# Optimization experiments

Measured on AMD Instinct MI355X. Metric: run time of the kernel, lower is better.

## Reference

```python
import jax, jax.numpy as jnp
import numpy as np

B, F, V, E = 16384, 39, 100000, 16
D0, D1, D2 = 32, 32, 32

def setup_inputs() -> dict:
    key = jax.random.key(0)
    ks = jax.random.split(key, 12)
    return {
        "Xi": jax.random.randint(ks[0], (B, F, 1), 0, V),
        "Xv": jax.random.uniform(ks[1], (B, F), dtype=jnp.float32),
        "emb_tables": jax.random.normal(ks[2], (F, V, E), dtype=jnp.float32),
        "w_first": jax.random.normal(ks[3], (D0, F, E), dtype=jnp.float32),
        "w_inner": jax.random.normal(ks[4], (D0, F, E), dtype=jnp.float32),
        "lin1_W": jax.random.normal(ks[5], (D1, D0), dtype=jnp.float32) * 0.1,
        "lin1_b": jax.random.normal(ks[6], (D1,), dtype=jnp.float32) * 0.1,
        "lin2_W": jax.random.normal(ks[7], (D2, D1), dtype=jnp.float32) * 0.1,
        "lin2_b": jax.random.normal(ks[8], (D2,), dtype=jnp.float32) * 0.1,
        "last_W": jax.random.normal(ks[9], (1, D2), dtype=jnp.float32) * 0.1,
        "last_b": jax.random.normal(ks[10], (1,), dtype=jnp.float32) * 0.1,
    }

def reference(Xi, Xv, emb_tables, w_first, w_inner, lin1_W, lin1_b, lin2_W, lin2_b, last_W, last_b):
    idx = Xi[:, :, 0]                                  # [B,F]
    # per-field embedding gather, scaled by feature value
    emb = emb_tables[jnp.arange(F)[None, :], idx]      # [B,F,E]
    emb = emb * Xv[:, :, None]                         # [B,F,E]
    # first-order: nested loops over (D0, F) collapse to one einsum
    first = jnp.einsum('bfe,dfe->bd', emb, w_first)    # [B,D0]
    # inner-product second-order: (sum over fields of <emb_f, w_df>)^2
    s = jnp.einsum('bfe,dfe->bd', emb, w_inner)        # [B,D0]
    x = first + s * s
    # deep MLP (relu, no dropout/batchnorm in inference)
    x = jax.nn.relu(x @ lin1_W.T + lin1_b)
    x = jax.nn.relu(x @ lin2_W.T + lin2_b)
    x = x @ last_W.T + last_b                          # [B,1]
    return jnp.sum(x, axis=1)                          # [B]
```

## Files before the change

### kernel.cpp

```cpp
#include <hip/hip_runtime.h>


namespace {

typedef _Float16 half8 __attribute__((ext_vector_type(8)));
typedef float floatx4 __attribute__((ext_vector_type(4)));

constexpr int Bn = 16384;
constexpr int Fn = 39;
constexpr int Vn = 100000;
constexpr int En = 16;
constexpr int M = 32;
constexpr int KST = 20;
constexpr int NRT = Bn / 16;
constexpr int WBLOCKS = 20;
constexpr int AWS_OFF_H = 65536;

__device__ __forceinline__ half8 cvt8s(float4 a, float4 b, float s) {
    half8 h;
    h[0] = (_Float16)(a.x * s); h[1] = (_Float16)(a.y * s);
    h[2] = (_Float16)(a.z * s); h[3] = (_Float16)(a.w * s);
    h[4] = (_Float16)(b.x * s); h[5] = (_Float16)(b.y * s);
    h[6] = (_Float16)(b.z * s); h[7] = (_Float16)(b.w * s);
    return h;
}

__device__ __forceinline__ half8 cvt8(float4 a, float4 b) {
    half8 h;
    h[0] = (_Float16)a.x; h[1] = (_Float16)a.y;
    h[2] = (_Float16)a.z; h[3] = (_Float16)a.w;
    h[4] = (_Float16)b.x; h[5] = (_Float16)b.y;
    h[6] = (_Float16)b.z; h[7] = (_Float16)b.w;
    return h;
}

__global__ __launch_bounds__(256) void pnn_stage(
    const int* __restrict__ Xi,
    const float* __restrict__ Xv,
    const float* __restrict__ T,
    const float* __restrict__ w_first,
    const float* __restrict__ w_inner,
    _Float16* __restrict__ ws)
{
    _Float16* __restrict__ Wws = ws;
    _Float16* __restrict__ Aws = ws + AWS_OFF_H;

    const int tid = threadIdx.x;

    if (blockIdx.x >= NRT) {
        const int slot = (blockIdx.x - NRT) * 256 + tid;
        const int t16 = slot / (KST * 64);
        const int rem = slot % (KST * 64);
        const int t = rem >> 6;
        const int lane = rem & 63;
        const int n = t16 * 16 + (lane & 15);
        const int kb = t * 32 + (lane >> 4) * 8;
        half8 h = {0, 0, 0, 0, 0, 0, 0, 0};
        if (!(t == KST - 1 && (lane >> 4) >= 2)) {
            const float* src = ((n < 32) ? (w_first + (size_t)n * 624)
                                         : (w_inner + (size_t)(n - 32) * 624)) + kb;
            const float4 a = *reinterpret_cast<const float4*>(src);
            const float4 b = *reinterpret_cast<const float4*>(src + 4);
            h = cvt8(a, b);
        }
        *reinterpret_cast<half8*>(Wws + (size_t)slot * 8) = h;
        return;
    }

    __shared__ _Float16 At[KST * 512];
    __shared__ int   xi[624];
    __shared__ float xv[624];

    const int rt = blockIdx.x;
    const int r0 = rt * 16;

    if (tid < 156) {
        reinterpret_cast<int4*>(xi)[tid] =
            reinterpret_cast<const int4*>(Xi + (size_t)r0 * Fn)[tid];
        reinterpret_cast<float4*>(xv)[tid] =
            reinterpret_cast<const float4*>(Xv + (size_t)r0 * Fn)[tid];
    }
    if (tid < 32) {
        half8 z = {0, 0, 0, 0, 0, 0, 0, 0};
        *reinterpret_cast<half8*>(At + ((KST - 1) * 64 + 32 + tid) * 8) = z;
    }
    __syncthreads();

    for (int i = tid; i < 624; i += 256) {
        const int r = i & 15, f = i >> 4;
        const int idx = xi[r * Fn + f];
        const float s = xv[r * Fn + f];
        const float4* src = reinterpret_cast<const float4*>(
            T + ((size_t)f * Vn + (size_t)idx) * En);
        const float4 q0 = src[0], q1 = src[1], q2 = src[2], q3 = src[3];
        const int base = (((f >> 1) * 64) + (f & 1) * 32 + r) * 8;
        *reinterpret_cast<half8*>(At + base)       = cvt8s(q0, q1, s);
        *reinterpret_cast<half8*>(At + base + 128) = cvt8s(q2, q3, s);
    }
    __syncthreads();

    const int4* s4 = reinterpret_cast<const int4*>(At);
    int4* d4 = reinterpret_cast<int4*>(Aws + (size_t)rt * KST * 512);
#pragma unroll
    for (int j = 0; j < 5; ++j) d4[tid + j * 256] = s4[tid + j * 256];
}

struct SMemE {
    float x[M * 69];
    float wsh[2176];
    float r1[1024];
    float r2[1024];
};

__global__ __launch_bounds__(512) void pnn_gemm(
    const _Float16* __restrict__ ws,
    const float* __restrict__ lin1_W,
    const float* __restrict__ lin1_b,
    const float* __restrict__ lin2_W,
    const float* __restrict__ lin2_b,
    const float* __restrict__ last_W,
    const float* __restrict__ last_b,
    float* __restrict__ out)
{
    __shared__ SMemE sm;

    const _Float16* __restrict__ Wws = ws;
    const _Float16* __restrict__ Aws = ws + AWS_OFF_H;

    const int tid = threadIdx.x;
    const int lane = tid & 63;
    const int wv = tid >> 6;
    const int q = wv & 1;
    const int t16 = wv >> 1;
    const int row0 = blockIdx.x * M;

    const _Float16* aptr = Aws + ((size_t)(blockIdx.x * 2 + q) * KST) * 512 + lane * 8;
    const _Float16* bptr = Wws + ((size_t)t16 * KST) * 512 + lane * 8;

    floatx4 acc = {0.0f, 0.0f, 0.0f, 0.0f};
#pragma unroll
    for (int t = 0; t < KST; ++t) {
        const half8 af = *reinterpret_cast<const half8*>(aptr + t * 512);
        const half8 bf = *reinterpret_cast<const half8*>(bptr + t * 512);
        acc = __builtin_amdgcn_mfma_f32_16x16x32_f16(af, bf, acc, 0, 0, 0);
    }

    {
        const int col = t16 * 16 + (lane & 15);
        const int rbase = q * 16 + (lane >> 4) * 4;
#pragma unroll
        for (int r = 0; r < 4; ++r)
            sm.x[(rbase + r) * 69 + col] = acc[r];
    }

    for (int i = tid; i < 2145; i += 512) {
        float v;
        if (i < 1024)      v = lin1_W[i];
        else if (i < 2048) v = lin2_W[i - 1024];
        else if (i < 2080) v = lin1_b[i - 2048];
        else if (i < 2112) v = lin2_b[i - 2080];
        else if (i < 2144) v = last_W[i - 2112];
        else               v = last_b[0];
        sm.wsh[i] = v;
    }
    __syncthreads();

    for (int p = tid; p < 1024; p += 512) {
        const int j = p >> 5, r = p & 31;
        const float fi = sm.x[r * 69 + j];
        const float s  = sm.x[r * 69 + 32 + j];
        sm.r1[j * 32 + r] = fi + s * s;
    }
    __syncthreads();

    {
        const int r = tid & 31, n0 = (tid >> 5) * 2;
        float a0 = sm.wsh[2048 + n0];
        float a1 = sm.wsh[2048 + n0 + 1];
#pragma unroll
        for (int j = 0; j < 32; ++j) {
            const float xj = sm.r1[j * 32 + r];
            a0 = fmaf(sm.wsh[n0 * 32 + j],       xj, a0);
            a1 = fmaf(sm.wsh[(n0 + 1) * 32 + j], xj, a1);
        }
        sm.r2[n0 * 32 + r]       = fmaxf(a0, 0.0f);
        sm.r2[(n0 + 1) * 32 + r] = fmaxf(a1, 0.0f);
    }
    __syncthreads();

    {
        const int r = tid & 31, n0 = (tid >> 5) * 2;
        float a0 = sm.wsh[2080 + n0];
        float a1 = sm.wsh[2080 + n0 + 1];
#pragma unroll
        for (int j = 0; j < 32; ++j) {
            const float xj = sm.r2[j * 32 + r];
            a0 = fmaf(sm.wsh[1024 + n0 * 32 + j],       xj, a0);
            a1 = fmaf(sm.wsh[1024 + (n0 + 1) * 32 + j], xj, a1);
        }
        sm.r1[n0 * 32 + r]       = fmaxf(a0, 0.0f);
        sm.r1[(n0 + 1) * 32 + r] = fmaxf(a1, 0.0f);
    }
    __syncthreads();

    if (tid < M) {
        float res = sm.wsh[2144];
#pragma unroll
        for (int j = 0; j < 32; ++j)
            res = fmaf(sm.wsh[2112 + j], sm.r1[j * 32 + tid], res);
        out[row0 + tid] = res;
    }
}

}

extern "C" void kernel_launch(void* const* d_in, const int* in_sizes, int n_in,
                              void* d_out, int out_size, void* d_ws, size_t ws_size,
                              hipStream_t stream) {
    (void)in_sizes; (void)n_in; (void)out_size; (void)ws_size;
    const int*   Xi      = (const int*)d_in[0];
    const float* Xv      = (const float*)d_in[1];
    const float* T       = (const float*)d_in[2];
    const float* w_first = (const float*)d_in[3];
    const float* w_inner = (const float*)d_in[4];
    const float* lin1_W  = (const float*)d_in[5];
    const float* lin1_b  = (const float*)d_in[6];
    const float* lin2_W  = (const float*)d_in[7];
    const float* lin2_b  = (const float*)d_in[8];
    const float* last_W  = (const float*)d_in[9];
    const float* last_b  = (const float*)d_in[10];
    float* out = (float*)d_out;
    _Float16* ws = (_Float16*)d_ws;

    hipLaunchKernelGGL(pnn_stage, dim3(NRT + WBLOCKS), dim3(256), 0, stream,
                       Xi, Xv, T, w_first, w_inner, ws);
    hipLaunchKernelGGL(pnn_gemm, dim3(Bn / M), dim3(512), 0, stream,
                       ws, lin1_W, lin1_b, lin2_W, lin2_b, last_W, last_b, out);
}
```

Before: 330.4 us.

## Gather embeddings one thread per (row, field) writing directly to workspace

Replaces the per-16-row block that staged the embedding gather through shared memory with a flat grid where each thread handles one (batch row, field) pair and writes its scaled fp16 fragments straight into the MFMA-ready workspace layout. Table reads use nontemporal loads, and the zero padding of the last K step moves into separate zero-fill blocks. This removes the shared-memory staging, the barriers and the limited per-block parallelism. In exchange the Xi/Xv reads are strided across threads and the global stores are scattered 16-byte writes.

```diff
diff --git a/kernel.cpp b/kernel.cpp
--- a/kernel.cpp
+++ b/kernel.cpp
@@ -5,6 +5,7 @@
 
 typedef _Float16 half8 __attribute__((ext_vector_type(8)));
 typedef float floatx4 __attribute__((ext_vector_type(4)));
+typedef float f32x4 __attribute__((ext_vector_type(4)));
 
 constexpr int Bn = 16384;
 constexpr int Fn = 39;
@@ -12,18 +13,11 @@
 constexpr int En = 16;
 constexpr int M = 32;
 constexpr int KST = 20;
-constexpr int NRT = Bn / 16;
+constexpr int AWS_OFF_H = 65536;
+
+constexpr int GB = (Bn * Fn) / 256;
 constexpr int WBLOCKS = 20;
-constexpr int AWS_OFF_H = 65536;
-
-__device__ __forceinline__ half8 cvt8s(float4 a, float4 b, float s) {
-    half8 h;
-    h[0] = (_Float16)(a.x * s); h[1] = (_Float16)(a.y * s);
-    h[2] = (_Float16)(a.z * s); h[3] = (_Float16)(a.w * s);
-    h[4] = (_Float16)(b.x * s); h[5] = (_Float16)(b.y * s);
-    h[6] = (_Float16)(b.z * s); h[7] = (_Float16)(b.w * s);
-    return h;
-}
+constexpr int ZBLOCKS = 128;
 
 __device__ __forceinline__ half8 cvt8(float4 a, float4 b) {
     half8 h;
@@ -31,6 +25,15 @@
     h[2] = (_Float16)a.z; h[3] = (_Float16)a.w;
     h[4] = (_Float16)b.x; h[5] = (_Float16)b.y;
     h[6] = (_Float16)b.z; h[7] = (_Float16)b.w;
+    return h;
+}
+
+__device__ __forceinline__ half8 cvt8s(f32x4 a, f32x4 b, float s) {
+    half8 h;
+    h[0] = (_Float16)(a[0] * s); h[1] = (_Float16)(a[1] * s);
+    h[2] = (_Float16)(a[2] * s); h[3] = (_Float16)(a[3] * s);
+    h[4] = (_Float16)(b[0] * s); h[5] = (_Float16)(b[1] * s);
+    h[6] = (_Float16)(b[2] * s); h[7] = (_Float16)(b[3] * s);
     return h;
 }
 
@@ -46,63 +49,55 @@
     _Float16* __restrict__ Aws = ws + AWS_OFF_H;
 
     const int tid = threadIdx.x;
-
-    if (blockIdx.x >= NRT) {
-        const int slot = (blockIdx.x - NRT) * 256 + tid;
-        const int t16 = slot / (KST * 64);
-        const int rem = slot % (KST * 64);
-        const int t = rem >> 6;
-        const int lane = rem & 63;
-        const int n = t16 * 16 + (lane & 15);
-        const int kb = t * 32 + (lane >> 4) * 8;
-        half8 h = {0, 0, 0, 0, 0, 0, 0, 0};
-        if (!(t == KST - 1 && (lane >> 4) >= 2)) {
-            const float* src = ((n < 32) ? (w_first + (size_t)n * 624)
-                                         : (w_inner + (size_t)(n - 32) * 624)) + kb;
-            const float4 a = *reinterpret_cast<const float4*>(src);
-            const float4 b = *reinterpret_cast<const float4*>(src + 4);
-            h = cvt8(a, b);
+    const int blk = blockIdx.x;
+
+    if (blk >= GB) {
+        if (blk < GB + WBLOCKS) {
+            const int slot = (blk - GB) * 256 + tid;
+            const int t16 = slot / (KST * 64);
+            const int rem = slot % (KST * 64);
+            const int t = rem >> 6;
+            const int lane = rem & 63;
+            const int n = t16 * 16 + (lane & 15);
+            const int kb = t * 32 + (lane >> 4) * 8;
+            half8 h = {0, 0, 0, 0, 0, 0, 0, 0};
+            if (!(t == KST - 1 && (lane >> 4) >= 2)) {
+                const float* src = ((n < 32) ? (w_first + (size_t)n * 624)
+                                             : (w_inner + (size_t)(n - 32) * 624)) + kb;
+                const float4 a = *reinterpret_cast<const float4*>(src);
+                const float4 b = *reinterpret_cast<const float4*>(src + 4);
+                h = cvt8(a, b);
+            }
+            *reinterpret_cast<half8*>(Wws + (size_t)slot * 8) = h;
+        } else {
+            const int j = (blk - GB - WBLOCKS) * 256 + tid;
+            const int rt = j >> 5, s = j & 31;
+            half8 z = {0, 0, 0, 0, 0, 0, 0, 0};
+            *reinterpret_cast<half8*>(
+                Aws + (size_t)rt * (KST * 512) + (KST - 1) * 512 + 256 + s * 8) = z;
         }
-        *reinterpret_cast<half8*>(Wws + (size_t)slot * 8) = h;
         return;
     }
 
-    __shared__ _Float16 At[KST * 512];
-    __shared__ int   xi[624];
-    __shared__ float xv[624];
-
-    const int rt = blockIdx.x;
-    const int r0 = rt * 16;
-
-    if (tid < 156) {
-        reinterpret_cast<int4*>(xi)[tid] =
-            reinterpret_cast<const int4*>(Xi + (size_t)r0 * Fn)[tid];
-        reinterpret_cast<float4*>(xv)[tid] =
-            reinterpret_cast<const float4*>(Xv + (size_t)r0 * Fn)[tid];
-    }
-    if (tid < 32) {
-        half8 z = {0, 0, 0, 0, 0, 0, 0, 0};
-        *reinterpret_cast<half8*>(At + ((KST - 1) * 64 + 32 + tid) * 8) = z;
-    }
-    __syncthreads();
-
-    for (int i = tid; i < 624; i += 256) {
-        const int r = i & 15, f = i >> 4;
-        const int idx = xi[r * Fn + f];
-        const float s = xv[r * Fn + f];
-        const float4* src = reinterpret_cast<const float4*>(
-            T + ((size_t)f * Vn + (size_t)idx) * En);
-        const float4 q0 = src[0], q1 = src[1], q2 = src[2], q3 = src[3];
-        const int base = (((f >> 1) * 64) + (f & 1) * 32 + r) * 8;
-        *reinterpret_cast<half8*>(At + base)       = cvt8s(q0, q1, s);
-        *reinterpret_cast<half8*>(At + base + 128) = cvt8s(q2, q3, s);
-    }
-    __syncthreads();
-
-    const int4* s4 = reinterpret_cast<const int4*>(At);
-    int4* d4 = reinterpret_cast<int4*>(Aws + (size_t)rt * KST * 512);
-#pragma unroll
-    for (int j = 0; j < 5; ++j) d4[tid + j * 256] = s4[tid + j * 256];
+    const int g = blk * 256 + tid;
+    const int b = g & (Bn - 1);
+    const int f = g >> 14;
+
+    const int idx = Xi[b * Fn + f];
+    const float s = Xv[b * Fn + f];
+
+    const f32x4* src = reinterpret_cast<const f32x4*>(
+        T + ((size_t)f * Vn + (size_t)idx) * En);
+    const f32x4 q0 = __builtin_nontemporal_load(src);
+    const f32x4 q1 = __builtin_nontemporal_load(src + 1);
+    const f32x4 q2 = __builtin_nontemporal_load(src + 2);
+    const f32x4 q3 = __builtin_nontemporal_load(src + 3);
+
+    const int rt = b >> 4, r = b & 15;
+    _Float16* dst = Aws + (size_t)rt * (KST * 512)
+                    + (f >> 1) * 512 + (f & 1) * 256 + r * 8;
+    *reinterpret_cast<half8*>(dst)       = cvt8s(q0, q1, s);
+    *reinterpret_cast<half8*>(dst + 128) = cvt8s(q2, q3, s);
 }
 
 struct SMemE {
@@ -168,8 +163,8 @@
     for (int p = tid; p < 1024; p += 512) {
         const int j = p >> 5, r = p & 31;
         const float fi = sm.x[r * 69 + j];
-        const float s  = sm.x[r * 69 + 32 + j];
-        sm.r1[j * 32 + r] = fi + s * s;
+        const float sq = sm.x[r * 69 + 32 + j];
+        sm.r1[j * 32 + r] = fi + sq * sq;
     }
     __syncthreads();
 
@@ -232,7 +227,7 @@
     float* out = (float*)d_out;
     _Float16* ws = (_Float16*)d_ws;
 
-    hipLaunchKernelGGL(pnn_stage, dim3(NRT + WBLOCKS), dim3(256), 0, stream,
+    hipLaunchKernelGGL(pnn_stage, dim3(GB + WBLOCKS + ZBLOCKS), dim3(256), 0, stream,
                        Xi, Xv, T, w_first, w_inner, ws);
     hipLaunchKernelGGL(pnn_gemm, dim3(Bn / M), dim3(512), 0, stream,
                        ws, lin1_W, lin1_b, lin2_W, lin2_b, last_W, last_b, out);
```

After: 338.1 us. 2.3% more time.
